# Optimization experiments

Measured on AMD Instinct MI355X. Metric: run time of the kernel, lower is better.

The kernel has to match this reference:

```python
import jax, jax.numpy as jnp
import numpy as np

N, E = 50000, 400000
IN, HID, OUT = 256, 192, 128  # hidden = floor((128+256)/2) = 192


def setup_inputs() -> dict:
    key = jax.random.key(0)
    ks = jax.random.split(key, 8)
    def glorot(k, fi, fo):
        lim = (6.0 / (fi + fo)) ** 0.5
        return jax.random.uniform(k, (fi, fo), jnp.float32, -lim, lim)
    return {
        "x": jax.random.normal(ks[0], (N, IN), jnp.float32),
        "edge_index": jax.random.randint(ks[1], (2, E), 0, N, jnp.int64),
        "W1": glorot(ks[2], IN, HID),  "b1": jnp.zeros((HID,), jnp.float32),
        "W2": glorot(ks[3], HID, HID), "b2": jnp.zeros((HID,), jnp.float32),
        "W3": glorot(ks[4], HID, OUT), "b3": jnp.zeros((OUT,), jnp.float32),
    }


def gcn_conv(x, src, dst, norm, W, b, n):
    # PyG GCNConv: out = D^-1/2 (A+I) D^-1/2 (x W) + b
    h = x @ W                               # [N, Fout]
    msg = h[src] * norm[:, None]            # [E+N, Fout] gathered, normalized messages
    return jax.ops.segment_sum(msg, dst, num_segments=n) + b


def reference(x, edge_index, W1, b1, W2, b2, W3, b3):
    n = x.shape[0]
    loops = jnp.arange(n, dtype=edge_index.dtype)
    src = jnp.concatenate([edge_index[0], loops])  # add self-loops
    dst = jnp.concatenate([edge_index[1], loops])
    deg = jax.ops.segment_sum(jnp.ones_like(dst, dtype=x.dtype), dst, num_segments=n)
    dinv = jnp.where(deg > 0, deg ** -0.5, 0.0)
    norm = dinv[src] * dinv[dst]            # [E+N]

    h = jax.nn.relu(gcn_conv(x, src, dst, norm, W1, b1, n))
    h = jax.nn.relu(gcn_conv(h, src, dst, norm, W2, b2, n))
    h = jax.nn.sigmoid(gcn_conv(h, src, dst, norm, W3, b3, n))
    # vectorized replacement of the per-element Python threshold loop
    h_clone = jnp.where(h >= 0.5, 1.0, 0.0).astype(h.dtype)
    return h, h_clone
```

## Files before the change

kernel.cpp:

```cpp
#include <hip/hip_runtime.h>
#include <math.h>

constexpr int Nn   = 50000;
constexpr int Ee   = 400000;
constexpr int FIN  = 256;
constexpr int FHID = 192;
constexpr int FOUT = 128;

typedef float    f32x4 __attribute__((ext_vector_type(4)));
typedef _Float16 f16x8 __attribute__((ext_vector_type(8)));

__device__ inline f32x4 mfma16(f16x8 a, f16x8 b, f32x4 c) {
    return __builtin_amdgcn_mfma_f32_16x16x32_f16(a, b, c, 0, 0, 0);
}


__global__ void init_cnt_k(int* cnt, int n) {
    int i = blockIdx.x * blockDim.x + threadIdx.x;
    if (i < n) cnt[i] = 0;
}

__global__ void detect_k(const long long* p, int n, int* flag) {
    if (threadIdx.x == 0 && blockIdx.x == 0) {
        int ok = 1;
        for (int i = 0; i < 16; i++) {
            long long v = p[i];
            if (v < 0 || v >= n) ok = 0;
        }
        *flag = ok;
    }
}

__global__ void conv_k(const void* edge, const int* flag, int* srcI, int* dstI,
                       int* cnt, int ne) {
    int e = blockIdx.x * blockDim.x + threadIdx.x;
    if (e >= ne) return;
    int s, d;
    if (*flag) {
        const long long* p = (const long long*)edge;
        s = (int)p[e];
        d = (int)p[ne + e];
    } else {
        const int* p = (const int*)edge;
        s = p[e];
        d = p[ne + e];
    }
    srcI[e] = s;
    dstI[e] = d;
    atomicAdd(&cnt[d], 1);
}

__global__ void dinv_k(const int* cnt, float* dinv, int n) {
    int i = blockIdx.x * blockDim.x + threadIdx.x;
    if (i < n) dinv[i] = 1.0f / sqrtf((float)(cnt[i] + 1));
}

__global__ __launch_bounds__(256) void scan1_k(const int* cnt, int n, int* rowptr,
                                               int* blockSum) {
    __shared__ int sm[256];
    int b = blockIdx.x, tid = threadIdx.x;
    int gbase = b * 1024 + tid * 4;
    int v[4];
#pragma unroll
    for (int j = 0; j < 4; j++) v[j] = (gbase + j < n) ? cnt[gbase + j] : 0;
    int tsum = v[0] + v[1] + v[2] + v[3];
    sm[tid] = tsum;
    __syncthreads();
    for (int off = 1; off < 256; off <<= 1) {
        int t = (tid >= off) ? sm[tid - off] : 0;
        __syncthreads();
        sm[tid] += t;
        __syncthreads();
    }
    int excl = sm[tid] - tsum;
#pragma unroll
    for (int j = 0; j < 4; j++) {
        if (gbase + j < n) rowptr[gbase + j] = excl;
        excl += v[j];
    }
    if (tid == 255) blockSum[b] = sm[255];
}

__global__ void scan2_k(const int* blockSum, int nb, int* blockOff) {
    if (threadIdx.x == 0 && blockIdx.x == 0) {
        int run = 0;
        for (int b = 0; b < nb; b++) { blockOff[b] = run; run += blockSum[b]; }
        blockOff[nb] = run;
    }
}

__global__ void scan3_k(int* rowptr, const int* blockOff, int* cursor, int n, int nb) {
    int i = blockIdx.x * blockDim.x + threadIdx.x;
    if (i < n) {
        int r = rowptr[i] + blockOff[i >> 10];
        rowptr[i] = r;
        cursor[i] = r;
    }
    if (i == 0) rowptr[n] = blockOff[nb];
}

__global__ void place_k(const int* srcI, const int* dstI, const float* dinv,
                        int* cursor, int* esrc, float* enorm, int ne) {
    int e = blockIdx.x * blockDim.x + threadIdx.x;
    if (e >= ne) return;
    int s = srcI[e], d = dstI[e];
    int pos = atomicAdd(&cursor[d], 1);
    esrc[pos] = s;
    enorm[pos] = dinv[s] * dinv[d];
}

__global__ void split_w_k(const float* __restrict__ W, _Float16* __restrict__ wh,
                          _Float16* __restrict__ wl, int K, int F) {
    int idx = blockIdx.x * blockDim.x + threadIdx.x;
    if (idx >= K * F) return;
    int k = idx / F, f = idx - k * F;
    float w = W[idx];
    _Float16 h = (_Float16)w;
    float d = w - (float)h;
    wh[(size_t)f * K + k] = h;
    wl[(size_t)f * K + k] = (_Float16)(d * 4096.f);
}

template <int K, int F, int NR, int MODE>
__global__ __launch_bounds__(256) void gemm_mfma(
    const float* __restrict__ inF, const _Float16* __restrict__ inH,
    const _Float16* __restrict__ inL, const _Float16* __restrict__ whi,
    const _Float16* __restrict__ wlo, float* __restrict__ out, int M) {
    const int tid  = threadIdx.x;
    const int wid  = tid >> 6;
    const int lane = tid & 63;
    const int l15  = lane & 15;
    const int l4   = lane >> 4;
    const int rb   = blockIdx.x * 128 + wid * 32;
    const int cb   = blockIdx.y * (NR * 16);

    f32x4 accH[2][NR], accL[2][NR];
#pragma unroll
    for (int mi = 0; mi < 2; mi++)
#pragma unroll
        for (int ni = 0; ni < NR; ni++)
#pragma unroll
            for (int r = 0; r < 4; r++) { accH[mi][ni][r] = 0.f; accL[mi][ni][r] = 0.f; }

    for (int k0 = 0; k0 < K; k0 += 32) {
        const int kk = k0 + l4 * 8;
        f16x8 ah[2], al[2];
#pragma unroll
        for (int mi = 0; mi < 2; mi++) {
            const int row = rb + mi * 16 + l15;
            if constexpr (MODE == 0) {
                if (row < M) {
                    const float* p = inF + (size_t)row * K + kk;
                    float4 f0 = *(const float4*)p;
                    float4 f1 = *(const float4*)(p + 4);
                    float v[8] = {f0.x, f0.y, f0.z, f0.w, f1.x, f1.y, f1.z, f1.w};
#pragma unroll
                    for (int j = 0; j < 8; j++) {
                        _Float16 h = (_Float16)v[j];
                        float d = v[j] - (float)h;
                        ah[mi][j] = h;
                        al[mi][j] = (_Float16)(d * 4096.f);
                    }
                } else {
#pragma unroll
                    for (int j = 0; j < 8; j++) { ah[mi][j] = (_Float16)0.f; al[mi][j] = (_Float16)0.f; }
                }
            } else {
                if (row < M) {
                    ah[mi] = *(const f16x8*)(inH + (size_t)row * K + kk);
                    al[mi] = *(const f16x8*)(inL + (size_t)row * K + kk);
                } else {
#pragma unroll
                    for (int j = 0; j < 8; j++) { ah[mi][j] = (_Float16)0.f; al[mi][j] = (_Float16)0.f; }
                }
            }
        }
#pragma unroll
        for (int ni = 0; ni < NR; ni++) {
            const int col = cb + ni * 16 + l15;
            f16x8 bh = *(const f16x8*)(whi + (size_t)col * K + kk);
            f16x8 bl = *(const f16x8*)(wlo + (size_t)col * K + kk);
#pragma unroll
            for (int mi = 0; mi < 2; mi++) {
                accH[mi][ni] = mfma16(ah[mi], bh, accH[mi][ni]);
                accL[mi][ni] = mfma16(ah[mi], bl, accL[mi][ni]);
                accL[mi][ni] = mfma16(al[mi], bh, accL[mi][ni]);
            }
        }
    }
#pragma unroll
    for (int mi = 0; mi < 2; mi++)
#pragma unroll
        for (int r = 0; r < 4; r++) {
            const int row = rb + mi * 16 + l4 * 4 + r;
            if (row < M) {
#pragma unroll
                for (int ni = 0; ni < NR; ni++) {
                    const int col = cb + ni * 16 + l15;
                    out[(size_t)row * F + col] =
                        accH[mi][ni][r] + accL[mi][ni][r] * (1.f / 4096.f);
                }
            }
        }
}

template <int F, int WS>
__global__ void agg2_k(const float* __restrict__ h, const float* __restrict__ dinv,
                       const int* __restrict__ rowptr, const int* __restrict__ esrc,
                       const float* __restrict__ enorm, const float* __restrict__ bias,
                       _Float16* __restrict__ ah, _Float16* __restrict__ al,
                       float* __restrict__ outf, int n) {
    constexpr int FV = F / 64;
    int wid = (blockIdx.x * blockDim.x + threadIdx.x) >> 6;
    int lane = threadIdx.x & 63;
    if (wid >= n) return;
    int i = wid;
    float di = dinv[i];
    const float* hrow = h + (size_t)i * F;
    float acc[FV];
#pragma unroll
    for (int j = 0; j < FV; j++) acc[j] = di * di * hrow[lane + 64 * j];
    int e0 = rowptr[i], e1 = rowptr[i + 1];
    for (int e = e0; e < e1; e++) {
        int s = esrc[e];
        float w = enorm[e];
        const float* hs = h + (size_t)s * F;
#pragma unroll
        for (int j = 0; j < FV; j++) acc[j] += w * hs[lane + 64 * j];
    }
#pragma unroll
    for (int j = 0; j < FV; j++) {
        int c = lane + 64 * j;
        if constexpr (WS == 1) {
            float a = fmaxf(acc[j] + bias[c], 0.f);
            _Float16 hh = (_Float16)a;
            float d = a - (float)hh;
            ah[(size_t)i * F + c] = hh;
            al[(size_t)i * F + c] = (_Float16)(d * 4096.f);
        } else {
            outf[(size_t)i * F + c] = acc[j];
        }
    }
}

__global__ void final_k(const float* __restrict__ agg, const float* __restrict__ b3,
                        float* __restrict__ outh, float* __restrict__ outc, int total4) {
    int idx = blockIdx.x * blockDim.x + threadIdx.x;
    if (idx >= total4) return;
    int c4 = idx & 31;
    float4 v = ((const float4*)agg)[idx];
    float4 b = ((const float4*)b3)[c4];
    float4 s;
    s.x = 1.f / (1.f + expf(-(v.x + b.x)));
    s.y = 1.f / (1.f + expf(-(v.y + b.y)));
    s.z = 1.f / (1.f + expf(-(v.z + b.z)));
    s.w = 1.f / (1.f + expf(-(v.w + b.w)));
    ((float4*)outh)[idx] = s;
    float4 t;
    t.x = s.x >= 0.5f ? 1.f : 0.f;
    t.y = s.y >= 0.5f ? 1.f : 0.f;
    t.z = s.z >= 0.5f ? 1.f : 0.f;
    t.w = s.w >= 0.5f ? 1.f : 0.f;
    ((float4*)outc)[idx] = t;
}

extern "C" void kernel_launch(void* const* d_in, const int* in_sizes, int n_in,
                              void* d_out, int out_size, void* d_ws, size_t ws_size,
                              hipStream_t stream) {
    const float* x  = (const float*)d_in[0];
    const void*  ei = d_in[1];
    const float* W1 = (const float*)d_in[2];
    const float* b1 = (const float*)d_in[3];
    const float* W2 = (const float*)d_in[4];
    const float* b2 = (const float*)d_in[5];
    const float* W3 = (const float*)d_in[6];
    const float* b3 = (const float*)d_in[7];
    float* out = (float*)d_out;

    char* w = (char*)d_ws;
    size_t off = 0;
    auto alloc = [&](size_t bytes) -> void* {
        off = (off + 255) & ~(size_t)255;
        void* p = w + off;
        off += bytes;
        return p;
    };
    float*     bufA = (float*)alloc((size_t)Nn * FHID * 4);
    _Float16*  Ph   = (_Float16*)alloc((size_t)Nn * FHID * 2 * 2);
    _Float16*  Pl   = Ph + (size_t)Nn * FHID;
    float*     Pf   = (float*)Ph;
    int*   srcI   = (int*)alloc((size_t)Ee * 4);
    int*   dstI   = (int*)alloc((size_t)Ee * 4);
    int*   esrc   = (int*)alloc((size_t)Ee * 4);
    float* enorm  = (float*)alloc((size_t)Ee * 4);
    int*   cnt    = (int*)alloc((size_t)Nn * 4);
    float* dinv   = (float*)alloc((size_t)Nn * 4);
    int*   rowptr = (int*)alloc((size_t)(Nn + 1) * 4);
    int*   cursor = (int*)alloc((size_t)Nn * 4);
    int*   blockSum = (int*)alloc(64 * 4);
    int*   blockOff = (int*)alloc(65 * 4);
    int*   flag   = (int*)alloc(4);
    _Float16* w1h = (_Float16*)alloc((size_t)FIN * FHID * 2);
    _Float16* w1l = (_Float16*)alloc((size_t)FIN * FHID * 2);
    _Float16* w2h = (_Float16*)alloc((size_t)FHID * FHID * 2);
    _Float16* w2l = (_Float16*)alloc((size_t)FHID * FHID * 2);
    _Float16* w3h = (_Float16*)alloc((size_t)FHID * FOUT * 2);
    _Float16* w3l = (_Float16*)alloc((size_t)FHID * FOUT * 2);

    const int NB = (Nn + 1023) / 1024;
    const int gN = (Nn + 255) / 256;
    const int gE = (Ee + 255) / 256;

    init_cnt_k<<<gN, 256, 0, stream>>>(cnt, Nn);
    detect_k<<<1, 64, 0, stream>>>((const long long*)ei, Nn, flag);
    conv_k<<<gE, 256, 0, stream>>>(ei, flag, srcI, dstI, cnt, Ee);
    dinv_k<<<gN, 256, 0, stream>>>(cnt, dinv, Nn);
    scan1_k<<<NB, 256, 0, stream>>>(cnt, Nn, rowptr, blockSum);
    scan2_k<<<1, 64, 0, stream>>>(blockSum, NB, blockOff);
    scan3_k<<<gN, 256, 0, stream>>>(rowptr, blockOff, cursor, Nn, NB);
    place_k<<<gE, 256, 0, stream>>>(srcI, dstI, dinv, cursor, esrc, enorm, Ee);

    split_w_k<<<(FIN * FHID + 255) / 256, 256, 0, stream>>>(W1, w1h, w1l, FIN, FHID);
    split_w_k<<<(FHID * FHID + 255) / 256, 256, 0, stream>>>(W2, w2h, w2l, FHID, FHID);
    split_w_k<<<(FHID * FOUT + 255) / 256, 256, 0, stream>>>(W3, w3h, w3l, FHID, FOUT);

    const int gRows = (Nn + 127) / 128;
    const int gAgg  = (Nn * 64 + 255) / 256;

    gemm_mfma<FIN, FHID, 6, 0><<<dim3(gRows, 2), 256, 0, stream>>>(
        x, nullptr, nullptr, w1h, w1l, bufA, Nn);
    agg2_k<FHID, 1><<<gAgg, 256, 0, stream>>>(bufA, dinv, rowptr, esrc, enorm,
                                              b1, Ph, Pl, nullptr, Nn);
    gemm_mfma<FHID, FHID, 6, 2><<<dim3(gRows, 2), 256, 0, stream>>>(
        nullptr, Ph, Pl, w2h, w2l, bufA, Nn);
    agg2_k<FHID, 1><<<gAgg, 256, 0, stream>>>(bufA, dinv, rowptr, esrc, enorm,
                                              b2, Ph, Pl, nullptr, Nn);
    gemm_mfma<FHID, FOUT, 4, 2><<<dim3(gRows, 2), 256, 0, stream>>>(
        nullptr, Ph, Pl, w3h, w3l, bufA, Nn);
    agg2_k<FOUT, 0><<<gAgg, 256, 0, stream>>>(bufA, dinv, rowptr, esrc, enorm,
                                              nullptr, nullptr, nullptr, Pf, Nn);
    const int total4 = Nn * FOUT / 4;
    final_k<<<(total4 + 255) / 256, 256, 0, stream>>>(Pf, b3, out,
                                                      out + (size_t)Nn * FOUT, total4);
}
```

Before: 495.9 us.

## Double-buffer GEMM loads, retile warps, unroll edge gather, fuse sigmoid epilogue

The MFMA GEMM becomes a software-pipelined loop that prefetches the next K-slice of A and B into registers while the current one is consumed. Its block tiling changes to 2x2 warps over 64 rows, and edge rows are clamped instead of branched on. The aggregation kernel unrolls the neighbour loop by four to keep more independent gathers in flight. The final sigmoid/threshold step is fused into the last aggregation, which removes a kernel launch and a round trip through the intermediate buffer. Register pressure rises from the double-buffered sets and may lower occupancy.

```diff
diff --git a/kernel.cpp b/kernel.cpp
--- a/kernel.cpp
+++ b/kernel.cpp
@@ -121,18 +121,89 @@
     wl[(size_t)f * K + k] = (_Float16)(d * 4096.f);
 }
 
+template <int NR, int MODE>
+struct KSet {
+    f16x8  bh[NR], bl[NR];
+    f16x8  ah[2], al[2];
+    float4 ar[2][2];
+};
+
 template <int K, int F, int NR, int MODE>
-__global__ __launch_bounds__(256) void gemm_mfma(
+__device__ inline void load_set(KSet<NR, MODE>& S, int kk,
+                                const float* __restrict__ inF,
+                                const _Float16* __restrict__ inH,
+                                const _Float16* __restrict__ inL,
+                                const _Float16* __restrict__ whi,
+                                const _Float16* __restrict__ wlo,
+                                int r0, int r1, int cb, int l15) {
+#pragma unroll
+    for (int ni = 0; ni < NR; ni++) {
+        const size_t boff = (size_t)(cb + ni * 16 + l15) * K + kk;
+        S.bh[ni] = *(const f16x8*)(whi + boff);
+        S.bl[ni] = *(const f16x8*)(wlo + boff);
+    }
+    if constexpr (MODE == 0) {
+        const float* p0 = inF + (size_t)r0 * K + kk;
+        const float* p1 = inF + (size_t)r1 * K + kk;
+        S.ar[0][0] = *(const float4*)p0;
+        S.ar[0][1] = *(const float4*)(p0 + 4);
+        S.ar[1][0] = *(const float4*)p1;
+        S.ar[1][1] = *(const float4*)(p1 + 4);
+    } else {
+        S.ah[0] = *(const f16x8*)(inH + (size_t)r0 * K + kk);
+        S.al[0] = *(const f16x8*)(inL + (size_t)r0 * K + kk);
+        S.ah[1] = *(const f16x8*)(inH + (size_t)r1 * K + kk);
+        S.al[1] = *(const f16x8*)(inL + (size_t)r1 * K + kk);
+    }
+}
+
+__device__ inline void split8(float4 f0, float4 f1, f16x8& h, f16x8& l) {
+    float v[8] = {f0.x, f0.y, f0.z, f0.w, f1.x, f1.y, f1.z, f1.w};
+#pragma unroll
+    for (int j = 0; j < 8; j++) {
+        _Float16 hh = (_Float16)v[j];
+        h[j] = hh;
+        l[j] = (_Float16)((v[j] - (float)hh) * 4096.f);
+    }
+}
+
+template <int NR, int MODE>
+__device__ inline void consume_set(KSet<NR, MODE>& S, f32x4 (&accH)[2][NR],
+                                   f32x4 (&accL)[2][NR]) {
+    f16x8 ah[2], al[2];
+    if constexpr (MODE == 0) {
+        split8(S.ar[0][0], S.ar[0][1], ah[0], al[0]);
+        split8(S.ar[1][0], S.ar[1][1], ah[1], al[1]);
+    } else {
+        ah[0] = S.ah[0]; al[0] = S.al[0];
+        ah[1] = S.ah[1]; al[1] = S.al[1];
+    }
+#pragma unroll
+    for (int ni = 0; ni < NR; ni++)
+#pragma unroll
+        for (int mi = 0; mi < 2; mi++) {
+            accH[mi][ni] = mfma16(ah[mi], S.bh[ni], accH[mi][ni]);
+            accL[mi][ni] = mfma16(ah[mi], S.bl[ni], accL[mi][ni]);
+            accL[mi][ni] = mfma16(al[mi], S.bh[ni], accL[mi][ni]);
+        }
+}
+
+template <int K, int F, int NR, int MODE>
+__global__ __launch_bounds__(256) void gemm_v2(
     const float* __restrict__ inF, const _Float16* __restrict__ inH,
     const _Float16* __restrict__ inL, const _Float16* __restrict__ whi,
     const _Float16* __restrict__ wlo, float* __restrict__ out, int M) {
     const int tid  = threadIdx.x;
-    const int wid  = tid >> 6;
     const int lane = tid & 63;
     const int l15  = lane & 15;
     const int l4   = lane >> 4;
-    const int rb   = blockIdx.x * 128 + wid * 32;
-    const int cb   = blockIdx.y * (NR * 16);
+    const int wid  = tid >> 6;
+    const int wrow = wid >> 1, wcol = wid & 1;
+    const int rb   = blockIdx.x * 64 + wrow * 32;
+    const int cb   = (blockIdx.y * 2 + wcol) * (NR * 16);
+    const int r0 = min(rb + l15, M - 1);
+    const int r1 = min(rb + 16 + l15, M - 1);
+    const int kbase = l4 * 8;
 
     f32x4 accH[2][NR], accL[2][NR];
 #pragma unroll
@@ -142,52 +213,17 @@
 #pragma unroll
             for (int r = 0; r < 4; r++) { accH[mi][ni][r] = 0.f; accL[mi][ni][r] = 0.f; }
 
-    for (int k0 = 0; k0 < K; k0 += 32) {
-        const int kk = k0 + l4 * 8;
-        f16x8 ah[2], al[2];
-#pragma unroll
-        for (int mi = 0; mi < 2; mi++) {
-            const int row = rb + mi * 16 + l15;
-            if constexpr (MODE == 0) {
-                if (row < M) {
-                    const float* p = inF + (size_t)row * K + kk;
-                    float4 f0 = *(const float4*)p;
-                    float4 f1 = *(const float4*)(p + 4);
-                    float v[8] = {f0.x, f0.y, f0.z, f0.w, f1.x, f1.y, f1.z, f1.w};
-#pragma unroll
-                    for (int j = 0; j < 8; j++) {
-                        _Float16 h = (_Float16)v[j];
-                        float d = v[j] - (float)h;
-                        ah[mi][j] = h;
-                        al[mi][j] = (_Float16)(d * 4096.f);
-                    }
-                } else {
-#pragma unroll
-                    for (int j = 0; j < 8; j++) { ah[mi][j] = (_Float16)0.f; al[mi][j] = (_Float16)0.f; }
-                }
-            } else {
-                if (row < M) {
-                    ah[mi] = *(const f16x8*)(inH + (size_t)row * K + kk);
-                    al[mi] = *(const f16x8*)(inL + (size_t)row * K + kk);
-                } else {
-#pragma unroll
-                    for (int j = 0; j < 8; j++) { ah[mi][j] = (_Float16)0.f; al[mi][j] = (_Float16)0.f; }
-                }
-            }
-        }
-#pragma unroll
-        for (int ni = 0; ni < NR; ni++) {
-            const int col = cb + ni * 16 + l15;
-            f16x8 bh = *(const f16x8*)(whi + (size_t)col * K + kk);
-            f16x8 bl = *(const f16x8*)(wlo + (size_t)col * K + kk);
-#pragma unroll
-            for (int mi = 0; mi < 2; mi++) {
-                accH[mi][ni] = mfma16(ah[mi], bh, accH[mi][ni]);
-                accL[mi][ni] = mfma16(ah[mi], bl, accL[mi][ni]);
-                accL[mi][ni] = mfma16(al[mi], bh, accL[mi][ni]);
-            }
-        }
-    }
+    KSet<NR, MODE> S0, S1;
+    load_set<K, F, NR, MODE>(S0, kbase, inF, inH, inL, whi, wlo, r0, r1, cb, l15);
+    for (int k0 = 0; k0 < K; k0 += 64) {
+        const int ka = (k0 + 32 < K) ? k0 + 32 : 0;
+        load_set<K, F, NR, MODE>(S1, ka + kbase, inF, inH, inL, whi, wlo, r0, r1, cb, l15);
+        consume_set<NR, MODE>(S0, accH, accL);
+        const int kb = (k0 + 64 < K) ? k0 + 64 : 0;
+        load_set<K, F, NR, MODE>(S0, kb + kbase, inF, inH, inL, whi, wlo, r0, r1, cb, l15);
+        consume_set<NR, MODE>(S1, accH, accL);
+    }
+
 #pragma unroll
     for (int mi = 0; mi < 2; mi++)
 #pragma unroll
@@ -209,19 +245,36 @@
                        const int* __restrict__ rowptr, const int* __restrict__ esrc,
                        const float* __restrict__ enorm, const float* __restrict__ bias,
                        _Float16* __restrict__ ah, _Float16* __restrict__ al,
-                       float* __restrict__ outf, int n) {
+                       float* __restrict__ outh, float* __restrict__ outc, int n) {
     constexpr int FV = F / 64;
-    int wid = (blockIdx.x * blockDim.x + threadIdx.x) >> 6;
+    int i = (blockIdx.x * blockDim.x + threadIdx.x) >> 6;
     int lane = threadIdx.x & 63;
-    if (wid >= n) return;
-    int i = wid;
+    if (i >= n) return;
     float di = dinv[i];
     const float* hrow = h + (size_t)i * F;
     float acc[FV];
 #pragma unroll
     for (int j = 0; j < FV; j++) acc[j] = di * di * hrow[lane + 64 * j];
-    int e0 = rowptr[i], e1 = rowptr[i + 1];
-    for (int e = e0; e < e1; e++) {
+    const int e1 = rowptr[i + 1];
+    int e = rowptr[i];
+    for (; e + 4 <= e1; e += 4) {
+        int s0 = esrc[e], s1 = esrc[e + 1], s2 = esrc[e + 2], s3 = esrc[e + 3];
+        float w0 = enorm[e], w1 = enorm[e + 1], w2 = enorm[e + 2], w3 = enorm[e + 3];
+        const float* p0 = h + (size_t)s0 * F;
+        const float* p1 = h + (size_t)s1 * F;
+        const float* p2 = h + (size_t)s2 * F;
+        const float* p3 = h + (size_t)s3 * F;
+#pragma unroll
+        for (int j = 0; j < FV; j++) {
+            int c = lane + 64 * j;
+            float v0 = p0[c], v1 = p1[c], v2 = p2[c], v3 = p3[c];
+            acc[j] += w0 * v0;
+            acc[j] += w1 * v1;
+            acc[j] += w2 * v2;
+            acc[j] += w3 * v3;
+        }
+    }
+    for (; e < e1; e++) {
         int s = esrc[e];
         float w = enorm[e];
         const float* hs = h + (size_t)s * F;
@@ -238,30 +291,11 @@
             ah[(size_t)i * F + c] = hh;
             al[(size_t)i * F + c] = (_Float16)(d * 4096.f);
         } else {
-            outf[(size_t)i * F + c] = acc[j];
-        }
-    }
-}
-
-__global__ void final_k(const float* __restrict__ agg, const float* __restrict__ b3,
-                        float* __restrict__ outh, float* __restrict__ outc, int total4) {
-    int idx = blockIdx.x * blockDim.x + threadIdx.x;
-    if (idx >= total4) return;
-    int c4 = idx & 31;
-    float4 v = ((const float4*)agg)[idx];
-    float4 b = ((const float4*)b3)[c4];
-    float4 s;
-    s.x = 1.f / (1.f + expf(-(v.x + b.x)));
-    s.y = 1.f / (1.f + expf(-(v.y + b.y)));
-    s.z = 1.f / (1.f + expf(-(v.z + b.z)));
-    s.w = 1.f / (1.f + expf(-(v.w + b.w)));
-    ((float4*)outh)[idx] = s;
-    float4 t;
-    t.x = s.x >= 0.5f ? 1.f : 0.f;
-    t.y = s.y >= 0.5f ? 1.f : 0.f;
-    t.z = s.z >= 0.5f ? 1.f : 0.f;
-    t.w = s.w >= 0.5f ? 1.f : 0.f;
-    ((float4*)outc)[idx] = t;
+            float s = 1.f / (1.f + expf(-(acc[j] + bias[c])));
+            outh[(size_t)i * F + c] = s;
+            outc[(size_t)i * F + c] = (s >= 0.5f) ? 1.f : 0.f;
+        }
+    }
 }
 
 extern "C" void kernel_launch(void* const* d_in, const int* in_sizes, int n_in,
@@ -286,9 +320,8 @@
         return p;
     };
     float*     bufA = (float*)alloc((size_t)Nn * FHID * 4);
-    _Float16*  Ph   = (_Float16*)alloc((size_t)Nn * FHID * 2 * 2);
-    _Float16*  Pl   = Ph + (size_t)Nn * FHID;
-    float*     Pf   = (float*)Ph;
+    _Float16*  Ph   = (_Float16*)alloc((size_t)Nn * FHID * 2);
+    _Float16*  Pl   = (_Float16*)alloc((size_t)Nn * FHID * 2);
     int*   srcI   = (int*)alloc((size_t)Ee * 4);
     int*   dstI   = (int*)alloc((size_t)Ee * 4);
     int*   esrc   = (int*)alloc((size_t)Ee * 4);
@@ -324,22 +357,20 @@
     split_w_k<<<(FHID * FHID + 255) / 256, 256, 0, stream>>>(W2, w2h, w2l, FHID, FHID);
     split_w_k<<<(FHID * FOUT + 255) / 256, 256, 0, stream>>>(W3, w3h, w3l, FHID, FOUT);
 
-    const int gRows = (Nn + 127) / 128;
+    const int gRows = (Nn + 63) / 64;
     const int gAgg  = (Nn * 64 + 255) / 256;
 
-    gemm_mfma<FIN, FHID, 6, 0><<<dim3(gRows, 2), 256, 0, stream>>>(
+    gemm_v2<FIN, FHID, 3, 0><<<dim3(gRows, 2), 256, 0, stream>>>(
         x, nullptr, nullptr, w1h, w1l, bufA, Nn);
     agg2_k<FHID, 1><<<gAgg, 256, 0, stream>>>(bufA, dinv, rowptr, esrc, enorm,
-                                              b1, Ph, Pl, nullptr, Nn);
-    gemm_mfma<FHID, FHID, 6, 2><<<dim3(gRows, 2), 256, 0, stream>>>(
+                                              b1, Ph, Pl, nullptr, nullptr, Nn);
+    gemm_v2<FHID, FHID, 3, 2><<<dim3(gRows, 2), 256, 0, stream>>>(
         nullptr, Ph, Pl, w2h, w2l, bufA, Nn);
     agg2_k<FHID, 1><<<gAgg, 256, 0, stream>>>(bufA, dinv, rowptr, esrc, enorm,
-                                              b2, Ph, Pl, nullptr, Nn);
-    gemm_mfma<FHID, FOUT, 4, 2><<<dim3(gRows, 2), 256, 0, stream>>>(
+                                              b2, Ph, Pl, nullptr, nullptr, Nn);
+    gemm_v2<FHID, FOUT, 2, 2><<<dim3(gRows, 2), 256, 0, stream>>>(
         nullptr, Ph, Pl, w3h, w3l, bufA, Nn);
     agg2_k<FOUT, 0><<<gAgg, 256, 0, stream>>>(bufA, dinv, rowptr, esrc, enorm,
-                                              nullptr, nullptr, nullptr, Pf, Nn);
-    const int total4 = Nn * FOUT / 4;
-    final_k<<<(total4 + 255) / 256, 256, 0, stream>>>(Pf, b3, out,
-                                                      out + (size_t)Nn * FOUT, total4);
-}
+                                              b3, nullptr, nullptr, out,
+                                              out + (size_t)Nn * FOUT, Nn);
+}
```

Measured after the change: 460.9 us. 7.1% less time.
